# Optimization experiments

Hardware: AMD Instinct MI355X
Metric: run time of the kernel (lower is better)

Reference implementation:

```python
import jax, jax.numpy as jnp
import numpy as np

N_NODES = 50000
N_EDGES = 800000
N_GRAPHS = 64
IN_DIM = 108
HID = 128
OUT_DIM = 64


def setup_inputs() -> dict:
    key = jax.random.key(0)
    ks = jax.random.split(key, 10)
    x = jax.random.normal(ks[0], (N_NODES, IN_DIM - 1), dtype=jnp.float32)
    votes = jax.random.normal(ks[1], (N_NODES, 1), dtype=jnp.float32)
    edge_index = jax.random.randint(ks[2], (2, N_EDGES), 0, N_NODES, dtype=jnp.int64)
    batch = jnp.sort(jax.random.randint(ks[3], (N_NODES,), 0, N_GRAPHS, dtype=jnp.int64))
    # SAGEConv params (PyG defaults: mean aggr; lin_l has bias, lin_r has no bias)
    s1 = 1.0 / np.sqrt(IN_DIM)
    s2 = 1.0 / np.sqrt(HID)
    W1l = jax.random.uniform(ks[4], (IN_DIM, HID), jnp.float32, -s1, s1)
    b1 = jnp.zeros((HID,), jnp.float32)
    W1r = jax.random.uniform(ks[5], (IN_DIM, HID), jnp.float32, -s1, s1)
    W2l = jax.random.uniform(ks[6], (HID, OUT_DIM), jnp.float32, -s2, s2)
    b2 = jnp.zeros((OUT_DIM,), jnp.float32)
    W2r = jax.random.uniform(ks[7], (HID, OUT_DIM), jnp.float32, -s2, s2)
    return {"x": x, "votes": votes, "edge_index": edge_index, "batch": batch,
            "W1l": W1l, "b1": b1, "W1r": W1r, "W2l": W2l, "b2": b2, "W2r": W2r}


def _sage_conv(h, src, dst, Wl, b, Wr):
    # mean-aggregate neighbor features x_j at target i, then lin_l(agg) + lin_r(x_i)
    agg = jax.ops.segment_sum(h[src], dst, num_segments=h.shape[0])  # [N, d]
    deg = jax.ops.segment_sum(jnp.ones((src.shape[0],), h.dtype), dst,
                              num_segments=h.shape[0])
    agg = agg / jnp.maximum(deg, 1.0)[:, None]
    return agg @ Wl + b + h @ Wr


def reference(x, votes, edge_index, batch, W1l, b1, W1r, W2l, b2, W2r):
    src, dst = edge_index[0], edge_index[1]
    h = jnp.concatenate([x, votes], axis=1)              # [N, 108]
    h = jax.nn.relu(_sage_conv(h, src, dst, W1l, b1, W1r))  # [N, 128]
    h = _sage_conv(h, src, dst, W2l, b2, W2r)               # [N, 64]
    return jax.ops.segment_max(h, batch, num_segments=N_GRAPHS)  # [G, 64]
```

## Files before the change

### kernel.cpp

```cpp
#include <hip/hip_runtime.h>
#include <hip/hip_bf16.h>

#define IN_F 108
#define XD   107
#define HID  128
#define OUTD 64
#define BSH 6
#define BNODES 64
#define MAXBK 1024
#define EPB 4096
#define SRCMASK 0x03FFFFFF
#define BP1_N (8 * 7 * 64 * 8)
#define BP2_N (8 * 4 * 64 * 8)

typedef unsigned short ushort_t;
typedef unsigned int uint_t;
typedef __attribute__((ext_vector_type(8))) short bf16x8;
typedef __attribute__((ext_vector_type(4))) float f32x4;

__device__ inline void atomicMaxF(float* addr, float val) {
    if (val >= 0.f) atomicMax((int*)addr, __float_as_int(val));
    else            atomicMin((unsigned int*)addr, __float_as_uint(val));
}

__device__ inline ushort_t f2bf(float f) {
    uint_t b = __float_as_uint(f);
    return (ushort_t)((b + 0x7fffu + ((b >> 16) & 1u)) >> 16);
}

__global__ void init0_kernel(int* bcnt, int nbk, float* out, int n) {
    int i = blockIdx.x * 256 + threadIdx.x;
    if (i < nbk) bcnt[i] = 0;
    if (i < n) out[i] = -__builtin_inff();
}

__global__ __launch_bounds__(256) void setup_kernel(
        const int* __restrict__ dst, int* __restrict__ bcnt, int E, int nbk, int nebl,
        const float* __restrict__ x, const float* __restrict__ votes,
        const float* __restrict__ W1l, const float* __restrict__ W1r,
        const float* __restrict__ W2l, const float* __restrict__ W2r,
        ushort_t* __restrict__ xb, ushort_t* __restrict__ bp1,
        ushort_t* __restrict__ bp2, int N) {
    __shared__ int lh[MAXBK];
    if ((int)blockIdx.x < nebl) {
        for (int i = threadIdx.x; i < nbk; i += 256) lh[i] = 0;
        __syncthreads();
        int base = blockIdx.x * EPB;
        int end = min(base + EPB, E);
        for (int k = base + threadIdx.x; k < end; k += 256)
            atomicAdd(&lh[dst[k] >> BSH], 1);
        __syncthreads();
        for (int i = threadIdx.x; i < nbk; i += 256)
            if (lh[i] > 0) atomicAdd(&bcnt[i], lh[i]);
        return;
    }
    int idx = ((int)blockIdx.x - nebl) * 256 + threadIdx.x;
    if (idx < N * IN_F) {
        int n = idx / IN_F, f = idx - n * IN_F;
        float v = (f < XD) ? x[n * XD + f] : votes[n];
        xb[idx] = f2bf(v);
    }
    if (idx < BP1_N) {
        int j = idx & 7;
        int lane = (idx >> 3) & 63;
        int rest = idx >> 9;
        int ks = rest % 7;
        int ct = rest / 7;
        int k = ks * 32 + (lane >> 4) * 8 + j;
        int col = ct * 16 + (lane & 15);
        float v = 0.f;
        if (k < IN_F) v = W1l[k * HID + col];
        else if (k < 2 * IN_F) v = W1r[(k - IN_F) * HID + col];
        bp1[idx] = f2bf(v);
    }
    int i2 = idx - BP1_N;
    if (i2 >= 0 && i2 < BP2_N) {
        int j = i2 & 7;
        int lane = (i2 >> 3) & 63;
        int ks = (i2 >> 9) & 3;
        int ct = i2 >> 11;
        int k = ks * 32 + (lane >> 4) * 8 + j;
        int col = ct * 16 + (lane & 15);
        float v = (col < OUTD) ? W2l[k * OUTD + col] : W2r[k * OUTD + (col - OUTD)];
        bp2[i2] = f2bf(v);
    }
}

__global__ __launch_bounds__(64) void bscan_kernel(const int* __restrict__ bcnt,
                                                   int* __restrict__ bbase,
                                                   int* __restrict__ brsv,
                                                   int* __restrict__ row_start,
                                                   int nbk, int N, int E) {
    int lane = threadIdx.x;
    int carry = 0;
    for (int b = 0; b < nbk; b += 64) {
        int i = b + lane;
        int orig = (i < nbk) ? bcnt[i] : 0;
        int v = orig;
#pragma unroll
        for (int d = 1; d < 64; d <<= 1) {
            int t = __shfl_up(v, d);
            if (lane >= d) v += t;
        }
        if (i < nbk) {
            int ex = carry + v - orig;
            bbase[i] = ex;
            brsv[i] = ex;
        }
        carry += __shfl(v, 63);
    }
    if (lane == 0) {
        bbase[nbk] = E;
        row_start[N] = E;
    }
}

__global__ __launch_bounds__(256) void bscatter_kernel(const int* __restrict__ src,
                                                       const int* __restrict__ dst,
                                                       int* __restrict__ brsv,
                                                       uint_t* __restrict__ ebuf,
                                                       int E, int nbk) {
    __shared__ int lh[MAXBK];
    __shared__ int lofs[MAXBK];
    for (int i = threadIdx.x; i < nbk; i += 256) lh[i] = 0;
    __syncthreads();
    int base = blockIdx.x * EPB;
    int end = min(base + EPB, E);
    for (int k = base + threadIdx.x; k < end; k += 256)
        atomicAdd(&lh[dst[k] >> BSH], 1);
    __syncthreads();
    for (int i = threadIdx.x; i < nbk; i += 256)
        if (lh[i] > 0) lofs[i] = atomicAdd(&brsv[i], lh[i]);
    __syncthreads();
    for (int k = base + threadIdx.x; k < end; k += 256) {
        int d = dst[k];
        int pos = atomicAdd(&lofs[d >> BSH], 1);
        ebuf[pos] = (uint_t)src[k] | ((uint_t)(d & (BNODES - 1)) << 26);
    }
}

__global__ __launch_bounds__(256) void bbuild_kernel(const uint_t* __restrict__ ebuf,
                                                     const int* __restrict__ bbase,
                                                     int* __restrict__ row_start,
                                                     int* __restrict__ sorted_src,
                                                     int N) {
    __shared__ int nh[BNODES];
    __shared__ int cur[BNODES];
    int b = blockIdx.x;
    int e0 = bbase[b], e1 = bbase[b + 1];
    int nlo = b << BSH;
    int nloc = min(BNODES, N - nlo);
    if (threadIdx.x < BNODES) nh[threadIdx.x] = 0;
    __syncthreads();
    for (int k = e0 + threadIdx.x; k < e1; k += 256)
        atomicAdd(&nh[ebuf[k] >> 26], 1);
    __syncthreads();
    if (threadIdx.x < 64) {
        int lane = threadIdx.x;
        int orig = nh[lane];
        int v = orig;
#pragma unroll
        for (int d = 1; d < 64; d <<= 1) {
            int t = __shfl_up(v, d);
            if (lane >= d) v += t;
        }
        int ex = e0 + v - orig;
        cur[lane] = ex;
        if (lane < nloc) row_start[nlo + lane] = ex;
    }
    __syncthreads();
    for (int k = e0 + threadIdx.x; k < e1; k += 256) {
        uint_t e = ebuf[k];
        int pos = atomicAdd(&cur[e >> 26], 1);
        sorted_src[pos] = (int)(e & SRCMASK);
    }
}

#define T1_M 32
#define A_STRIDE_US 232
#define A_STRIDE_U  116
#define H1_STRIDE_US 136
__global__ __launch_bounds__(256) void fused1_kernel(
        const ushort_t* __restrict__ xb,
        const int* __restrict__ row_start, const int* __restrict__ sorted_src,
        const ushort_t* __restrict__ bp1, const ushort_t* __restrict__ bp2,
        const float* __restrict__ b1, const float* __restrict__ b2,
        ushort_t* __restrict__ ub, float* __restrict__ vvb, int N) {
    __shared__ uint_t smem[T1_M * A_STRIDE_U];
    __shared__ int rsh[T1_M + 1];
    int n0 = blockIdx.x * T1_M;
    const uint_t* xbu = (const uint_t*)xb;

    for (int i = threadIdx.x; i < T1_M * 54; i += 256) {
        int m = i / 54, c = i - m * 54;
        int n = n0 + m;
        smem[m * A_STRIDE_U + 54 + c] = (n < N) ? xbu[n * 54 + c] : 0u;
    }
    for (int i = threadIdx.x; i < T1_M * 4; i += 256) {
        int m = i >> 2, c = i & 3;
        smem[m * A_STRIDE_U + 108 + c] = 0u;
    }
    if (threadIdx.x <= T1_M) {
        int n = n0 + threadIdx.x;
        rsh[threadIdx.x] = row_start[min(n, N)];
    }
    __syncthreads();

    int lane = threadIdx.x & 63;
    int wid  = threadIdx.x >> 6;
    int h  = lane >> 5;
    int l2 = lane & 31;

    int mq8 = wid * 8;
    int sl_next = 0;
    {
        int rs0 = rsh[mq8], re0 = rsh[mq8 + 1];
        if (re0 > rs0) {
            int c = min(64, re0 - rs0);
            sl_next = sorted_src[rs0 + min(lane, c - 1)];
        }
    }
    for (int it = 0; it < 8; ++it) {
        int m = mq8 + it;
        int rs = rsh[m], re = rsh[m + 1];
        int sl0 = sl_next;
        if (it < 7) {
            int rsn = rsh[m + 1], ren = rsh[m + 2];
            if (ren > rsn) {
                int c = min(64, ren - rsn);
                sl_next = sorted_src[rsn + min(lane, c - 1)];
            }
        }
        float a0 = 0.f, a1 = 0.f, a2 = 0.f, a3 = 0.f;
        for (int k0 = rs; k0 < re; k0 += 64) {
            int cnt = min(64, re - k0);
            int sl = (k0 == rs) ? sl0 : sorted_src[k0 + min(lane, cnt - 1)];
            int t = 0;
            for (; t + 8 <= cnt; t += 8) {
                int s0 = __shfl(sl, t + h);
                int s1 = __shfl(sl, t + 2 + h);
                int s2 = __shfl(sl, t + 4 + h);
                int s3 = __shfl(sl, t + 6 + h);
                if (l2 < 27) {
                    uint2 w0 = *(const uint2*)(xb + s0 * IN_F + 4 * l2);
                    uint2 w1 = *(const uint2*)(xb + s1 * IN_F + 4 * l2);
                    uint2 w2 = *(const uint2*)(xb + s2 * IN_F + 4 * l2);
                    uint2 w3 = *(const uint2*)(xb + s3 * IN_F + 4 * l2);
                    a0 += __uint_as_float(w0.x << 16) + __uint_as_float(w1.x << 16)
                        + __uint_as_float(w2.x << 16) + __uint_as_float(w3.x << 16);
                    a1 += __uint_as_float(w0.x & 0xffff0000u) + __uint_as_float(w1.x & 0xffff0000u)
                        + __uint_as_float(w2.x & 0xffff0000u) + __uint_as_float(w3.x & 0xffff0000u);
                    a2 += __uint_as_float(w0.y << 16) + __uint_as_float(w1.y << 16)
                        + __uint_as_float(w2.y << 16) + __uint_as_float(w3.y << 16);
                    a3 += __uint_as_float(w0.y & 0xffff0000u) + __uint_as_float(w1.y & 0xffff0000u)
                        + __uint_as_float(w2.y & 0xffff0000u) + __uint_as_float(w3.y & 0xffff0000u);
                }
            }
            for (; t < cnt; t += 2) {
                int tt = min(t + h, cnt - 1);
                int s = __shfl(sl, tt);
                if (t + h < cnt && l2 < 27) {
                    uint2 w = *(const uint2*)(xb + s * IN_F + 4 * l2);
                    a0 += __uint_as_float(w.x << 16);
                    a1 += __uint_as_float(w.x & 0xffff0000u);
                    a2 += __uint_as_float(w.y << 16);
                    a3 += __uint_as_float(w.y & 0xffff0000u);
                }
            }
        }
        a0 += __shfl_xor(a0, 32);
        a1 += __shfl_xor(a1, 32);
        a2 += __shfl_xor(a2, 32);
        a3 += __shfl_xor(a3, 32);
        int node = n0 + m;
        if (node < N && l2 < 27) {
            float inv = 1.f / fmaxf((float)(re - rs), 1.f);
            ushort4 p;
            p.x = f2bf(a0 * inv);
            p.y = f2bf(a1 * inv);
            p.z = f2bf(a2 * inv);
            p.w = f2bf(a3 * inv);
            *(ushort4*)((ushort_t*)smem + m * A_STRIDE_US + 4 * l2) = p;
        }
    }
    __syncthreads();

    int wrow = (wid & 1) << 4;
    int wcol = (wid >> 1) << 6;
    int arow = wrow + (lane & 15);
    int akoff = (lane >> 4) * 8;
    const ushort_t* sA = (const ushort_t*)smem;
    const bf16x8* bp1v = (const bf16x8*)bp1;

    f32x4 acc0 = {}, acc1 = {}, acc2_ = {}, acc3 = {};
    int ct0 = wcol >> 4;
#pragma unroll
    for (int ks = 0; ks < 7; ++ks) {
        bf16x8 af = *(const bf16x8*)(sA + arow * A_STRIDE_US + ks * 32 + akoff);
        bf16x8 bf0 = bp1v[((ct0 + 0) * 7 + ks) * 64 + lane];
        bf16x8 bf1 = bp1v[((ct0 + 1) * 7 + ks) * 64 + lane];
        bf16x8 bf2 = bp1v[((ct0 + 2) * 7 + ks) * 64 + lane];
        bf16x8 bf3 = bp1v[((ct0 + 3) * 7 + ks) * 64 + lane];
        acc0 = __builtin_amdgcn_mfma_f32_16x16x32_bf16(af, bf0, acc0, 0, 0, 0);
        acc1 = __builtin_amdgcn_mfma_f32_16x16x32_bf16(af, bf1, acc1, 0, 0, 0);
        acc2_ = __builtin_amdgcn_mfma_f32_16x16x32_bf16(af, bf2, acc2_, 0, 0, 0);
        acc3 = __builtin_amdgcn_mfma_f32_16x16x32_bf16(af, bf3, acc3, 0, 0, 0);
    }

    __syncthreads();
    ushort_t* sh1 = (ushort_t*)smem;
    {
        int colb = wcol + (lane & 15);
        int rowb = wrow + ((lane >> 4) << 2);
#pragma unroll
        for (int t = 0; t < 4; ++t) {
            f32x4 a = (t == 0) ? acc0 : (t == 1) ? acc1 : (t == 2) ? acc2_ : acc3;
            int col = colb + t * 16;
            float bj = b1[col];
#pragma unroll
            for (int r = 0; r < 4; ++r)
                sh1[(rowb + r) * H1_STRIDE_US + col] = f2bf(fmaxf(a[r] + bj, 0.f));
        }
    }
    __syncthreads();

    const bf16x8* bp2v = (const bf16x8*)bp2;
    f32x4 dcc0 = {}, dcc1 = {}, dcc2 = {}, dcc3 = {};
#pragma unroll
    for (int ks = 0; ks < 4; ++ks) {
        bf16x8 af = *(const bf16x8*)(sh1 + arow * H1_STRIDE_US + ks * 32 + akoff);
        bf16x8 bf0 = bp2v[((ct0 + 0) * 4 + ks) * 64 + lane];
        bf16x8 bf1 = bp2v[((ct0 + 1) * 4 + ks) * 64 + lane];
        bf16x8 bf2 = bp2v[((ct0 + 2) * 4 + ks) * 64 + lane];
        bf16x8 bf3 = bp2v[((ct0 + 3) * 4 + ks) * 64 + lane];
        dcc0 = __builtin_amdgcn_mfma_f32_16x16x32_bf16(af, bf0, dcc0, 0, 0, 0);
        dcc1 = __builtin_amdgcn_mfma_f32_16x16x32_bf16(af, bf1, dcc1, 0, 0, 0);
        dcc2 = __builtin_amdgcn_mfma_f32_16x16x32_bf16(af, bf2, dcc2, 0, 0, 0);
        dcc3 = __builtin_amdgcn_mfma_f32_16x16x32_bf16(af, bf3, dcc3, 0, 0, 0);
    }

    {
        int colb = wcol + (lane & 15);
        int rowb = wrow + ((lane >> 4) << 2);
#pragma unroll
        for (int t = 0; t < 4; ++t) {
            f32x4 a = (t == 0) ? dcc0 : (t == 1) ? dcc1 : (t == 2) ? dcc2 : dcc3;
            int col = colb + t * 16;
#pragma unroll
            for (int r = 0; r < 4; ++r) {
                int n = n0 + rowb + r;
                if (n < N) {
                    if (col < OUTD) {
                        ub[(n << 6) + col] = f2bf(a[r]);
                    } else {
                        vvb[(n << 6) + (col - OUTD)] = a[r] + b2[col - OUTD];
                    }
                }
            }
        }
    }
}

#define GF_NODES 64
__global__ __launch_bounds__(256) void gatherf_kernel(
        const ushort_t* __restrict__ ub,
        const int* __restrict__ row_start, const int* __restrict__ sorted_src,
        const float* __restrict__ vvb, const int* __restrict__ batch,
        float* __restrict__ out, int N) {
    int lane = threadIdx.x & 63;
    int wid = threadIdx.x >> 6;
    int nbase = blockIdx.x * GF_NODES + wid * 16;
    int g4 = lane >> 4;
    int l4 = lane & 15;
    int curg = -1;
    float m0 = 0.f, m1 = 0.f, m2 = 0.f, m3 = 0.f;
    for (int it = 0; it < 16; ++it) {
        int node = nbase + it;
        if (node >= N) break;
        int rs = row_start[node], re = row_start[node + 1];
        float a0 = 0.f, a1 = 0.f, a2 = 0.f, a3 = 0.f;
        for (int k0 = rs; k0 < re; k0 += 64) {
            int cnt = min(64, re - k0);
            int sl = sorted_src[k0 + min(lane, cnt - 1)];
            int t = 0;
            for (; t + 8 <= cnt; t += 8) {
                int s0 = __shfl(sl, t + g4);
                int s1 = __shfl(sl, t + 4 + g4);
                uint2 w0 = *(const uint2*)(ub + (s0 << 6) + 4 * l4);
                uint2 w1 = *(const uint2*)(ub + (s1 << 6) + 4 * l4);
                a0 += __uint_as_float(w0.x << 16) + __uint_as_float(w1.x << 16);
                a1 += __uint_as_float(w0.x & 0xffff0000u) + __uint_as_float(w1.x & 0xffff0000u);
                a2 += __uint_as_float(w0.y << 16) + __uint_as_float(w1.y << 16);
                a3 += __uint_as_float(w0.y & 0xffff0000u) + __uint_as_float(w1.y & 0xffff0000u);
            }
            for (; t < cnt; t += 4) {
                int tt = min(t + g4, cnt - 1);
                int s = __shfl(sl, tt);
                if (t + g4 < cnt) {
                    uint2 w = *(const uint2*)(ub + (s << 6) + 4 * l4);
                    a0 += __uint_as_float(w.x << 16);
                    a1 += __uint_as_float(w.x & 0xffff0000u);
                    a2 += __uint_as_float(w.y << 16);
                    a3 += __uint_as_float(w.y & 0xffff0000u);
                }
            }
        }
        a0 += __shfl_xor(a0, 16); a0 += __shfl_xor(a0, 32);
        a1 += __shfl_xor(a1, 16); a1 += __shfl_xor(a1, 32);
        a2 += __shfl_xor(a2, 16); a2 += __shfl_xor(a2, 32);
        a3 += __shfl_xor(a3, 16); a3 += __shfl_xor(a3, 32);
        if (lane < 16) {
            float inv = 1.f / fmaxf((float)(re - rs), 1.f);
            float4 vb = *(const float4*)(vvb + (node << 6) + 4 * l4);
            float h0v = a0 * inv + vb.x;
            float h1v = a1 * inv + vb.y;
            float h2v = a2 * inv + vb.z;
            float h3v = a3 * inv + vb.w;
            int g = batch[node];
            if (g != curg) {
                if (curg >= 0) {
                    float* o = out + (curg << 6) + 4 * l4;
                    atomicMaxF(o + 0, m0);
                    atomicMaxF(o + 1, m1);
                    atomicMaxF(o + 2, m2);
                    atomicMaxF(o + 3, m3);
                }
                curg = g;
                m0 = h0v; m1 = h1v; m2 = h2v; m3 = h3v;
            } else {
                m0 = fmaxf(m0, h0v);
                m1 = fmaxf(m1, h1v);
                m2 = fmaxf(m2, h2v);
                m3 = fmaxf(m3, h3v);
            }
        }
    }
    if (lane < 16 && curg >= 0) {
        float* o = out + (curg << 6) + 4 * l4;
        atomicMaxF(o + 0, m0);
        atomicMaxF(o + 1, m1);
        atomicMaxF(o + 2, m2);
        atomicMaxF(o + 3, m3);
    }
}

static inline size_t align256(size_t v) { return (v + 255) & ~(size_t)255; }

extern "C" void kernel_launch(void* const* d_in, const int* in_sizes, int n_in,
                              void* d_out, int out_size, void* d_ws, size_t ws_size,
                              hipStream_t stream) {
    const float* x     = (const float*)d_in[0];
    const float* votes = (const float*)d_in[1];
    const int*   eidx  = (const int*)d_in[2];
    const int*   batch = (const int*)d_in[3];
    const float* W1l   = (const float*)d_in[4];
    const float* b1    = (const float*)d_in[5];
    const float* W1r   = (const float*)d_in[6];
    const float* W2l   = (const float*)d_in[7];
    const float* b2    = (const float*)d_in[8];
    const float* W2r   = (const float*)d_in[9];
    float* out = (float*)d_out;

    const int N = in_sizes[1];
    const int E = in_sizes[2] / 2;
    const int* src = eidx;
    const int* dst = eidx + E;
    const int nbk = (N + BNODES - 1) >> BSH;

    char* ws = (char*)d_ws;
    size_t off = 0;
    int* bcnt       = (int*)(ws + off); off = align256(off + (size_t)nbk * 4);
    int* bbase      = (int*)(ws + off); off = align256(off + (size_t)(nbk + 1) * 4);
    int* brsv       = (int*)(ws + off); off = align256(off + (size_t)nbk * 4);
    int* row_start  = (int*)(ws + off); off = align256(off + (size_t)(N + 1) * 4);
    uint_t* ebuf    = (uint_t*)(ws + off); off = align256(off + (size_t)E * 4);
    int* sorted_src = (int*)(ws + off); off = align256(off + (size_t)E * 4);
    ushort_t* xb    = (ushort_t*)(ws + off); off = align256(off + (size_t)N * IN_F * 2);
    ushort_t* ub    = (ushort_t*)(ws + off); off = align256(off + (size_t)N * OUTD * 2);
    float* vvb      = (float*)(ws + off); off = align256(off + (size_t)N * OUTD * 4);
    ushort_t* bp1   = (ushort_t*)(ws + off); off = align256(off + (size_t)BP1_N * 2);
    ushort_t* bp2   = (ushort_t*)(ws + off); off = align256(off + (size_t)BP2_N * 2);

    {
        int mx = max(nbk, out_size);
        init0_kernel<<<(mx + 255) / 256, 256, 0, stream>>>(bcnt, nbk, out, out_size);
    }

    int nebl = (E + EPB - 1) / EPB;
    int prep_blocks = (N * IN_F + 255) / 256;
    setup_kernel<<<nebl + prep_blocks, 256, 0, stream>>>(dst, bcnt, E, nbk, nebl,
                                                         x, votes, W1l, W1r, W2l, W2r,
                                                         xb, bp1, bp2, N);

    bscan_kernel<<<1, 64, 0, stream>>>(bcnt, bbase, brsv, row_start, nbk, N, E);
    bscatter_kernel<<<nebl, 256, 0, stream>>>(src, dst, brsv, ebuf, E, nbk);
    bbuild_kernel<<<nbk, 256, 0, stream>>>(ebuf, bbase, row_start, sorted_src, N);

    fused1_kernel<<<(N + T1_M - 1) / T1_M, 256, 0, stream>>>(xb, row_start, sorted_src,
                                                             bp1, bp2, b1, b2, ub, vvb, N);
    gatherf_kernel<<<(N + GF_NODES - 1) / GF_NODES, 256, 0, stream>>>(
        ub, row_start, sorted_src, vvb, batch, out, N);
}
```

Measured before the change: 140.4 us.

## Switch features and MFMA to fp16 with packed half accumulation, shrink final gather blocks

```diff
diff --git a/kernel.cpp b/kernel.cpp
--- a/kernel.cpp
+++ b/kernel.cpp
@@ -15,7 +15,8 @@
 
 typedef unsigned short ushort_t;
 typedef unsigned int uint_t;
-typedef __attribute__((ext_vector_type(8))) short bf16x8;
+typedef _Float16 f16x8 __attribute__((ext_vector_type(8)));
+typedef _Float16 h2 __attribute__((ext_vector_type(2)));
 typedef __attribute__((ext_vector_type(4))) float f32x4;
 
 __device__ inline void atomicMaxF(float* addr, float val) {
@@ -23,9 +24,12 @@
     else            atomicMin((unsigned int*)addr, __float_as_uint(val));
 }
 
-__device__ inline ushort_t f2bf(float f) {
-    uint_t b = __float_as_uint(f);
-    return (ushort_t)((b + 0x7fffu + ((b >> 16) & 1u)) >> 16);
+__device__ inline ushort_t f2h_bits(float f) {
+    return __builtin_bit_cast(ushort_t, (_Float16)f);
+}
+
+__device__ inline h2 u_as_h2(uint_t u) {
+    return __builtin_bit_cast(h2, u);
 }
 
 __global__ void init0_kernel(int* bcnt, int nbk, float* out, int n) {
@@ -58,7 +62,7 @@
     if (idx < N * IN_F) {
         int n = idx / IN_F, f = idx - n * IN_F;
         float v = (f < XD) ? x[n * XD + f] : votes[n];
-        xb[idx] = f2bf(v);
+        xb[idx] = f2h_bits(v);
     }
     if (idx < BP1_N) {
         int j = idx & 7;
@@ -71,7 +75,7 @@
         float v = 0.f;
         if (k < IN_F) v = W1l[k * HID + col];
         else if (k < 2 * IN_F) v = W1r[(k - IN_F) * HID + col];
-        bp1[idx] = f2bf(v);
+        bp1[idx] = f2h_bits(v);
     }
     int i2 = idx - BP1_N;
     if (i2 >= 0 && i2 < BP2_N) {
@@ -82,7 +86,7 @@
         int k = ks * 32 + (lane >> 4) * 8 + j;
         int col = ct * 16 + (lane & 15);
         float v = (col < OUTD) ? W2l[k * OUTD + col] : W2r[k * OUTD + (col - OUTD)];
-        bp2[i2] = f2bf(v);
+        bp2[i2] = f2h_bits(v);
     }
 }
 
@@ -212,29 +216,14 @@
     int l2 = lane & 31;
 
     int mq8 = wid * 8;
-    int sl_next = 0;
-    {
-        int rs0 = rsh[mq8], re0 = rsh[mq8 + 1];
-        if (re0 > rs0) {
-            int c = min(64, re0 - rs0);
-            sl_next = sorted_src[rs0 + min(lane, c - 1)];
-        }
-    }
     for (int it = 0; it < 8; ++it) {
         int m = mq8 + it;
         int rs = rsh[m], re = rsh[m + 1];
-        int sl0 = sl_next;
-        if (it < 7) {
-            int rsn = rsh[m + 1], ren = rsh[m + 2];
-            if (ren > rsn) {
-                int c = min(64, ren - rsn);
-                sl_next = sorted_src[rsn + min(lane, c - 1)];
-            }
-        }
-        float a0 = 0.f, a1 = 0.f, a2 = 0.f, a3 = 0.f;
+        h2 c01 = {(_Float16)0.f, (_Float16)0.f};
+        h2 c23 = {(_Float16)0.f, (_Float16)0.f};
         for (int k0 = rs; k0 < re; k0 += 64) {
             int cnt = min(64, re - k0);
-            int sl = (k0 == rs) ? sl0 : sorted_src[k0 + min(lane, cnt - 1)];
+            int sl = sorted_src[k0 + min(lane, cnt - 1)];
             int t = 0;
             for (; t + 8 <= cnt; t += 8) {
                 int s0 = __shfl(sl, t + h);
@@ -246,14 +235,10 @@
                     uint2 w1 = *(const uint2*)(xb + s1 * IN_F + 4 * l2);
                     uint2 w2 = *(const uint2*)(xb + s2 * IN_F + 4 * l2);
                     uint2 w3 = *(const uint2*)(xb + s3 * IN_F + 4 * l2);
-                    a0 += __uint_as_float(w0.x << 16) + __uint_as_float(w1.x << 16)
-                        + __uint_as_float(w2.x << 16) + __uint_as_float(w3.x << 16);
-                    a1 += __uint_as_float(w0.x & 0xffff0000u) + __uint_as_float(w1.x & 0xffff0000u)
-                        + __uint_as_float(w2.x & 0xffff0000u) + __uint_as_float(w3.x & 0xffff0000u);
-                    a2 += __uint_as_float(w0.y << 16) + __uint_as_float(w1.y << 16)
-                        + __uint_as_float(w2.y << 16) + __uint_as_float(w3.y << 16);
-                    a3 += __uint_as_float(w0.y & 0xffff0000u) + __uint_as_float(w1.y & 0xffff0000u)
-                        + __uint_as_float(w2.y & 0xffff0000u) + __uint_as_float(w3.y & 0xffff0000u);
+                    c01 += u_as_h2(w0.x); c23 += u_as_h2(w0.y);
+                    c01 += u_as_h2(w1.x); c23 += u_as_h2(w1.y);
+                    c01 += u_as_h2(w2.x); c23 += u_as_h2(w2.y);
+                    c01 += u_as_h2(w3.x); c23 += u_as_h2(w3.y);
                 }
             }
             for (; t < cnt; t += 2) {
@@ -261,13 +246,13 @@
                 int s = __shfl(sl, tt);
                 if (t + h < cnt && l2 < 27) {
                     uint2 w = *(const uint2*)(xb + s * IN_F + 4 * l2);
-                    a0 += __uint_as_float(w.x << 16);
-                    a1 += __uint_as_float(w.x & 0xffff0000u);
-                    a2 += __uint_as_float(w.y << 16);
-                    a3 += __uint_as_float(w.y & 0xffff0000u);
+                    c01 += u_as_h2(w.x);
+                    c23 += u_as_h2(w.y);
                 }
             }
         }
+        float a0 = (float)c01[0], a1 = (float)c01[1];
+        float a2 = (float)c23[0], a3 = (float)c23[1];
         a0 += __shfl_xor(a0, 32);
         a1 += __shfl_xor(a1, 32);
         a2 += __shfl_xor(a2, 32);
@@ -276,10 +261,10 @@
         if (node < N && l2 < 27) {
             float inv = 1.f / fmaxf((float)(re - rs), 1.f);
             ushort4 p;
-            p.x = f2bf(a0 * inv);
-            p.y = f2bf(a1 * inv);
-            p.z = f2bf(a2 * inv);
-            p.w = f2bf(a3 * inv);
+            p.x = f2h_bits(a0 * inv);
+            p.y = f2h_bits(a1 * inv);
+            p.z = f2h_bits(a2 * inv);
+            p.w = f2h_bits(a3 * inv);
             *(ushort4*)((ushort_t*)smem + m * A_STRIDE_US + 4 * l2) = p;
         }
     }
@@ -290,21 +275,21 @@
     int arow = wrow + (lane & 15);
     int akoff = (lane >> 4) * 8;
     const ushort_t* sA = (const ushort_t*)smem;
-    const bf16x8* bp1v = (const bf16x8*)bp1;
+    const f16x8* bp1v = (const f16x8*)bp1;
 
     f32x4 acc0 = {}, acc1 = {}, acc2_ = {}, acc3 = {};
     int ct0 = wcol >> 4;
 #pragma unroll
     for (int ks = 0; ks < 7; ++ks) {
-        bf16x8 af = *(const bf16x8*)(sA + arow * A_STRIDE_US + ks * 32 + akoff);
-        bf16x8 bf0 = bp1v[((ct0 + 0) * 7 + ks) * 64 + lane];
-        bf16x8 bf1 = bp1v[((ct0 + 1) * 7 + ks) * 64 + lane];
-        bf16x8 bf2 = bp1v[((ct0 + 2) * 7 + ks) * 64 + lane];
-        bf16x8 bf3 = bp1v[((ct0 + 3) * 7 + ks) * 64 + lane];
-        acc0 = __builtin_amdgcn_mfma_f32_16x16x32_bf16(af, bf0, acc0, 0, 0, 0);
-        acc1 = __builtin_amdgcn_mfma_f32_16x16x32_bf16(af, bf1, acc1, 0, 0, 0);
-        acc2_ = __builtin_amdgcn_mfma_f32_16x16x32_bf16(af, bf2, acc2_, 0, 0, 0);
-        acc3 = __builtin_amdgcn_mfma_f32_16x16x32_bf16(af, bf3, acc3, 0, 0, 0);
+        f16x8 af = *(const f16x8*)(sA + arow * A_STRIDE_US + ks * 32 + akoff);
+        f16x8 bf0 = bp1v[((ct0 + 0) * 7 + ks) * 64 + lane];
+        f16x8 bf1 = bp1v[((ct0 + 1) * 7 + ks) * 64 + lane];
+        f16x8 bf2 = bp1v[((ct0 + 2) * 7 + ks) * 64 + lane];
+        f16x8 bf3 = bp1v[((ct0 + 3) * 7 + ks) * 64 + lane];
+        acc0 = __builtin_amdgcn_mfma_f32_16x16x32_f16(af, bf0, acc0, 0, 0, 0);
+        acc1 = __builtin_amdgcn_mfma_f32_16x16x32_f16(af, bf1, acc1, 0, 0, 0);
+        acc2_ = __builtin_amdgcn_mfma_f32_16x16x32_f16(af, bf2, acc2_, 0, 0, 0);
+        acc3 = __builtin_amdgcn_mfma_f32_16x16x32_f16(af, bf3, acc3, 0, 0, 0);
     }
 
     __syncthreads();
@@ -319,24 +304,24 @@
             float bj = b1[col];
 #pragma unroll
             for (int r = 0; r < 4; ++r)
-                sh1[(rowb + r) * H1_STRIDE_US + col] = f2bf(fmaxf(a[r] + bj, 0.f));
-        }
-    }
-    __syncthreads();
-
-    const bf16x8* bp2v = (const bf16x8*)bp2;
+                sh1[(rowb + r) * H1_STRIDE_US + col] = f2h_bits(fmaxf(a[r] + bj, 0.f));
+        }
+    }
+    __syncthreads();
+
+    const f16x8* bp2v = (const f16x8*)bp2;
     f32x4 dcc0 = {}, dcc1 = {}, dcc2 = {}, dcc3 = {};
 #pragma unroll
     for (int ks = 0; ks < 4; ++ks) {
-        bf16x8 af = *(const bf16x8*)(sh1 + arow * H1_STRIDE_US + ks * 32 + akoff);
-        bf16x8 bf0 = bp2v[((ct0 + 0) * 4 + ks) * 64 + lane];
-        bf16x8 bf1 = bp2v[((ct0 + 1) * 4 + ks) * 64 + lane];
-        bf16x8 bf2 = bp2v[((ct0 + 2) * 4 + ks) * 64 + lane];
-        bf16x8 bf3 = bp2v[((ct0 + 3) * 4 + ks) * 64 + lane];
-        dcc0 = __builtin_amdgcn_mfma_f32_16x16x32_bf16(af, bf0, dcc0, 0, 0, 0);
-        dcc1 = __builtin_amdgcn_mfma_f32_16x16x32_bf16(af, bf1, dcc1, 0, 0, 0);
-        dcc2 = __builtin_amdgcn_mfma_f32_16x16x32_bf16(af, bf2, dcc2, 0, 0, 0);
-        dcc3 = __builtin_amdgcn_mfma_f32_16x16x32_bf16(af, bf3, dcc3, 0, 0, 0);
+        f16x8 af = *(const f16x8*)(sh1 + arow * H1_STRIDE_US + ks * 32 + akoff);
+        f16x8 bf0 = bp2v[((ct0 + 0) * 4 + ks) * 64 + lane];
+        f16x8 bf1 = bp2v[((ct0 + 1) * 4 + ks) * 64 + lane];
+        f16x8 bf2 = bp2v[((ct0 + 2) * 4 + ks) * 64 + lane];
+        f16x8 bf3 = bp2v[((ct0 + 3) * 4 + ks) * 64 + lane];
+        dcc0 = __builtin_amdgcn_mfma_f32_16x16x32_f16(af, bf0, dcc0, 0, 0, 0);
+        dcc1 = __builtin_amdgcn_mfma_f32_16x16x32_f16(af, bf1, dcc1, 0, 0, 0);
+        dcc2 = __builtin_amdgcn_mfma_f32_16x16x32_f16(af, bf2, dcc2, 0, 0, 0);
+        dcc3 = __builtin_amdgcn_mfma_f32_16x16x32_f16(af, bf3, dcc3, 0, 0, 0);
     }
 
     {
@@ -351,7 +336,7 @@
                 int n = n0 + rowb + r;
                 if (n < N) {
                     if (col < OUTD) {
-                        ub[(n << 6) + col] = f2bf(a[r]);
+                        ub[(n << 6) + col] = f2h_bits(a[r]);
                     } else {
                         vvb[(n << 6) + (col - OUTD)] = a[r] + b2[col - OUTD];
                     }
@@ -361,7 +346,8 @@
     }
 }
 
-#define GF_NODES 64
+#define GF_NPW 4
+#define GF_NODES (4 * GF_NPW)
 __global__ __launch_bounds__(256) void gatherf_kernel(
         const ushort_t* __restrict__ ub,
         const int* __restrict__ row_start, const int* __restrict__ sorted_src,
@@ -369,16 +355,17 @@
         float* __restrict__ out, int N) {
     int lane = threadIdx.x & 63;
     int wid = threadIdx.x >> 6;
-    int nbase = blockIdx.x * GF_NODES + wid * 16;
+    int nbase = blockIdx.x * GF_NODES + wid * GF_NPW;
     int g4 = lane >> 4;
     int l4 = lane & 15;
     int curg = -1;
     float m0 = 0.f, m1 = 0.f, m2 = 0.f, m3 = 0.f;
-    for (int it = 0; it < 16; ++it) {
+    for (int it = 0; it < GF_NPW; ++it) {
         int node = nbase + it;
         if (node >= N) break;
         int rs = row_start[node], re = row_start[node + 1];
-        float a0 = 0.f, a1 = 0.f, a2 = 0.f, a3 = 0.f;
+        h2 c01 = {(_Float16)0.f, (_Float16)0.f};
+        h2 c23 = {(_Float16)0.f, (_Float16)0.f};
         for (int k0 = rs; k0 < re; k0 += 64) {
             int cnt = min(64, re - k0);
             int sl = sorted_src[k0 + min(lane, cnt - 1)];
@@ -388,23 +375,21 @@
                 int s1 = __shfl(sl, t + 4 + g4);
                 uint2 w0 = *(const uint2*)(ub + (s0 << 6) + 4 * l4);
                 uint2 w1 = *(const uint2*)(ub + (s1 << 6) + 4 * l4);
-                a0 += __uint_as_float(w0.x << 16) + __uint_as_float(w1.x << 16);
-                a1 += __uint_as_float(w0.x & 0xffff0000u) + __uint_as_float(w1.x & 0xffff0000u);
-                a2 += __uint_as_float(w0.y << 16) + __uint_as_float(w1.y << 16);
-                a3 += __uint_as_float(w0.y & 0xffff0000u) + __uint_as_float(w1.y & 0xffff0000u);
+                c01 += u_as_h2(w0.x); c23 += u_as_h2(w0.y);
+                c01 += u_as_h2(w1.x); c23 += u_as_h2(w1.y);
             }
             for (; t < cnt; t += 4) {
                 int tt = min(t + g4, cnt - 1);
                 int s = __shfl(sl, tt);
                 if (t + g4 < cnt) {
                     uint2 w = *(const uint2*)(ub + (s << 6) + 4 * l4);
-                    a0 += __uint_as_float(w.x << 16);
-                    a1 += __uint_as_float(w.x & 0xffff0000u);
-                    a2 += __uint_as_float(w.y << 16);
-                    a3 += __uint_as_float(w.y & 0xffff0000u);
+                    c01 += u_as_h2(w.x);
+                    c23 += u_as_h2(w.y);
                 }
             }
         }
+        float a0 = (float)c01[0], a1 = (float)c01[1];
+        float a2 = (float)c23[0], a3 = (float)c23[1];
         a0 += __shfl_xor(a0, 16); a0 += __shfl_xor(a0, 32);
         a1 += __shfl_xor(a1, 16); a1 += __shfl_xor(a1, 32);
         a2 += __shfl_xor(a2, 16); a2 += __shfl_xor(a2, 32);
```

Result: slower. 178.5 us (+27.2%).
